# Performance work log

Hardware: AMD Instinct MI355X
Metric: run time of the kernel (lower is better)

The kernel has to match this reference:

```python
import jax, jax.numpy as jnp
import numpy as np

N = 50000
E = 800000
G = 2500  # number of graphs


def setup_inputs() -> dict:
    key = jax.random.key(0)
    ks = jax.random.split(key, 10)
    x = jax.random.normal(ks[0], (N, 128), dtype=jnp.float32)
    edge_index = jax.random.randint(ks[1], (2, E), 0, N, dtype=jnp.int64)
    batch = jnp.sort(jax.random.randint(ks[2], (N,), 0, G, dtype=jnp.int64))
    def lin(k, fan_in, shape):
        return jax.random.normal(k, shape, dtype=jnp.float32) / np.sqrt(fan_in)
    return {
        'x': x, 'edge_index': edge_index, 'batch': batch,
        'W1': lin(ks[3], 128, (128, 64)), 'b1': jnp.zeros((64,), jnp.float32),
        'W2': lin(ks[4], 64, (64, 64)),  'b2': jnp.zeros((64,), jnp.float32),
        'W3': lin(ks[5], 64, (64, 64)),  'b3': jnp.zeros((64,), jnp.float32),
        'Wp1': lin(ks[6], 64, (64, 64)), 'bp1': jnp.zeros((64,), jnp.float32),
        'Wp2': lin(ks[7], 64, (64, 32)), 'bp2': jnp.zeros((32,), jnp.float32),
    }


def _gcn_norm(edge_index, n_nodes):
    # PyG GCNConv default: add self-loops, symmetric normalization
    loops = jnp.arange(n_nodes, dtype=edge_index.dtype)
    src = jnp.concatenate([edge_index[0], loops])
    dst = jnp.concatenate([edge_index[1], loops])
    deg = jax.ops.segment_sum(jnp.ones_like(dst, dtype=jnp.float32), dst,
                              num_segments=n_nodes)
    dis = jnp.where(deg > 0, jax.lax.rsqrt(deg), 0.0)
    norm = dis[src] * dis[dst]  # [E + N]
    return src, dst, norm


def _gcn_conv(x, W, b, src, dst, norm, n_nodes):
    h = x @ W                                   # transform first (small dim)
    m = h[src] * norm[:, None]                  # gather + scale
    out = jax.ops.segment_sum(m, dst, num_segments=n_nodes)  # scatter-add
    return out + b


def reference(x, edge_index, batch, W1, b1, W2, b2, W3, b3, Wp1, bp1, Wp2, bp2):
    n_nodes = x.shape[0]
    src, dst, norm = _gcn_norm(edge_index, n_nodes)
    x1 = jax.nn.relu(_gcn_conv(x, W1, b1, src, dst, norm, n_nodes))
    x2 = jax.nn.relu(_gcn_conv(x1, W2, b2, src, dst, norm, n_nodes))
    x3 = jax.nn.relu(_gcn_conv(x2, W3, b3, src, dst, norm, n_nodes))
    h = x1 + x2 + x3
    # global_mean_pool
    sums = jax.ops.segment_sum(h, batch, num_segments=G)
    counts = jax.ops.segment_sum(jnp.ones((n_nodes,), jnp.float32), batch,
                                 num_segments=G)
    pooled = sums / jnp.maximum(counts, 1.0)[:, None]
    z = jax.nn.relu(pooled @ Wp1 + bp1) @ Wp2 + bp2
    return z
```

## Files before the change

### kernel.cpp

```cpp
#include <hip/hip_runtime.h>
#include <math.h>


typedef short short8 __attribute__((ext_vector_type(8)));
typedef float f32x4 __attribute__((ext_vector_type(4)));

__device__ inline float bf2f(unsigned short h) {
    return __uint_as_float((unsigned)h << 16);
}
__device__ inline unsigned short f2bf(float f) {
    unsigned u = __float_as_uint(f);
    return (unsigned short)((u + (0x7FFFu + ((u >> 16) & 1u))) >> 16);
}
__device__ inline unsigned short f2h(float f) {
    union { _Float16 h; unsigned short u; } c;
    c.h = (_Float16)f;
    return c.u;
}
__device__ inline float h2f(unsigned short u) {
    union { unsigned short u; _Float16 h; } c;
    c.u = u;
    return (float)c.h;
}
__device__ inline void bh8f(short8 u, float4& a, float4& b) {
    a.x = bf2f((unsigned short)u[0]); a.y = bf2f((unsigned short)u[1]);
    a.z = bf2f((unsigned short)u[2]); a.w = bf2f((unsigned short)u[3]);
    b.x = bf2f((unsigned short)u[4]); b.y = bf2f((unsigned short)u[5]);
    b.z = bf2f((unsigned short)u[6]); b.w = bf2f((unsigned short)u[7]);
}
__device__ inline float4 f4fma(float s, float4 a, float4 acc) {
    acc.x += s * a.x; acc.y += s * a.y; acc.z += s * a.z; acc.w += s * a.w;
    return acc;
}

template <int K>
__global__ __launch_bounds__(256) void k_hist_gemm(const int* __restrict__ dst,
                                                   int* __restrict__ hist, int E, int chunk,
                                                   const float* __restrict__ X,
                                                   const float* __restrict__ W,
                                                   unsigned short* __restrict__ H, int n) {
    __shared__ int hh[256];
    __shared__ short wt[64 * K];
    int t = threadIdx.x;
    if (blockIdx.x < 256) {
        hh[t] = 0;
        __syncthreads();
        int e0 = blockIdx.x * chunk;
        int e1 = min(e0 + chunk, E);
        for (int e = e0 + t; e < e1; e += 256) atomicAdd(&hh[dst[e] >> 8], 1);
        __syncthreads();
        hist[blockIdx.x * 256 + t] = hh[t];
        return;
    }
    for (int idx = t; idx < 64 * K; idx += 256) {
        int k = idx >> 6, ch = idx & 63;
        wt[ch * K + k] = (short)f2bf(W[idx]);
    }
    __syncthreads();
    int wave = t >> 6, lane = t & 63;
    int q = lane >> 4, l = lane & 15;
    int tile = (blockIdx.x - 256) * 4 + wave;
    if (tile * 16 >= n) return;
    int node = tile * 16 + l;
    short8 afr[4][K / 32];
#pragma unroll
    for (int mb = 0; mb < 4; mb++)
#pragma unroll
        for (int s = 0; s < K / 32; s++)
            afr[mb][s] = *(const short8*)(wt + (mb * 16 + l) * K + s * 32 + q * 8);
    f32x4 acc[4] = {};
    const float* xr = X + (size_t)node * K + q * 8;
#pragma unroll
    for (int s = 0; s < K / 32; s++) {
        float4 xa = *(const float4*)(xr + s * 32);
        float4 xb = *(const float4*)(xr + s * 32 + 4);
        short8 bfr;
        bfr[0] = (short)f2bf(xa.x); bfr[1] = (short)f2bf(xa.y);
        bfr[2] = (short)f2bf(xa.z); bfr[3] = (short)f2bf(xa.w);
        bfr[4] = (short)f2bf(xb.x); bfr[5] = (short)f2bf(xb.y);
        bfr[6] = (short)f2bf(xb.z); bfr[7] = (short)f2bf(xb.w);
#pragma unroll
        for (int mb = 0; mb < 4; mb++)
            acc[mb] = __builtin_amdgcn_mfma_f32_16x16x32_bf16(afr[mb][s], bfr, acc[mb], 0, 0, 0);
    }
#pragma unroll
    for (int mb = 0; mb < 4; mb++) {
        ushort4 u;
        u.x = f2bf(acc[mb][0]); u.y = f2bf(acc[mb][1]);
        u.z = f2bf(acc[mb][2]); u.w = f2bf(acc[mb][3]);
        ((ushort4*)H)[(size_t)node * 16 + mb * 4 + q] = u;
    }
}

__global__ void kA_colscan(const int* __restrict__ hist, int* __restrict__ cursorA,
                           int* __restrict__ tot) {
    __shared__ int s[256];
    int t = threadIdx.x;
    int k = blockIdx.x;
    int v = hist[t * 256 + k];
    s[t] = v;
    __syncthreads();
    for (int st = 1; st < 256; st <<= 1) {
        int u = s[t];
        if (t >= st) u += s[t - st];
        __syncthreads();
        s[t] = u;
        __syncthreads();
    }
    cursorA[t * 256 + k] = s[t] - v;
    if (t == 255) tot[k] = s[255];
}

__global__ void kA_scatter(const int* __restrict__ src, const int* __restrict__ dst,
                           const int* __restrict__ cursorA, const int* __restrict__ tot,
                           unsigned* __restrict__ ebuf, int E, int chunk) {
    __shared__ int s[256];
    __shared__ int cur[256];
    int t = threadIdx.x;
    s[t] = tot[t];
    __syncthreads();
    for (int st = 1; st < 256; st <<= 1) {
        int u = s[t];
        if (t >= st) u += s[t - st];
        __syncthreads();
        s[t] = u;
        __syncthreads();
    }
    int bstart = (t == 0) ? 0 : s[t - 1];
    cur[t] = cursorA[blockIdx.x * 256 + t] + bstart;
    __syncthreads();
    int e0 = blockIdx.x * chunk;
    int e1 = min(e0 + chunk, E);
    for (int e = e0 + t; e < e1; e += 256) {
        int d = dst[e];
        int p = atomicAdd(&cur[d >> 8], 1);
        ebuf[p] = ((unsigned)(d & 255) << 24) | (unsigned)src[e];
    }
}

__global__ void kB1(const unsigned* __restrict__ ebuf, const int* __restrict__ tot,
                    float* __restrict__ dis, int* __restrict__ offsP, int N) {
    __shared__ int s[256];
    __shared__ int h[256];
    int t = threadIdx.x;
    int k = blockIdx.x;
    s[t] = tot[t];
    __syncthreads();
    for (int st = 1; st < 256; st <<= 1) {
        int u = s[t];
        if (t >= st) u += s[t - st];
        __syncthreads();
        s[t] = u;
        __syncthreads();
    }
    int lo = (k == 0) ? 0 : s[k - 1];
    int hi = s[k];
    int padbase = lo + 768 * k;
    h[t] = 0;
    __syncthreads();
    for (int p = lo + t; p < hi; p += 256) atomicAdd(&h[ebuf[p] >> 24], 1);
    __syncthreads();
    int c = h[t];
    int cp = (c + 3) & ~3;
    int node = k * 256 + t;
    if (node < N) dis[node] = rsqrtf((float)(c + 1));
    s[t] = cp;
    __syncthreads();
    for (int st = 1; st < 256; st <<= 1) {
        int u = s[t];
        if (t >= st) u += s[t - st];
        __syncthreads();
        s[t] = u;
        __syncthreads();
    }
    if (node < N) offsP[node] = ((padbase + s[t] - cp) << 9) | cp;
}

__global__ void kB2(const unsigned* __restrict__ ebuf, const int* __restrict__ tot,
                    const float* __restrict__ dis, const int* __restrict__ offsP,
                    unsigned* __restrict__ col, int N) {
    __shared__ int s[256];
    __shared__ int cur[256];
    int t = threadIdx.x;
    int k = blockIdx.x;
    s[t] = tot[t];
    __syncthreads();
    for (int st = 1; st < 256; st <<= 1) {
        int u = s[t];
        if (t >= st) u += s[t - st];
        __syncthreads();
        s[t] = u;
        __syncthreads();
    }
    int lo = (k == 0) ? 0 : s[k - 1];
    int hi = s[k];
    int node = k * 256 + t;
    int po = (node < N) ? offsP[node] : 0;
    cur[t] = po >> 9;
    __syncthreads();
    for (int p = lo + t; p < hi; p += 256) {
        unsigned e = ebuf[p];
        int srcI = (int)(e & 0x00FFFFFFu);
        int q = atomicAdd(&cur[e >> 24], 1);
        col[q] = ((unsigned)f2h(dis[srcI]) << 16) | (unsigned)srcI;
    }
    __syncthreads();
    if (node < N) {
        int end = (po >> 9) + (po & 511);
        for (int q = cur[t]; q < end; q++) col[q] = 0u;
    }
}

__global__ __launch_bounds__(256) void k_aggemm(const unsigned short* __restrict__ H,
                                                const unsigned* __restrict__ col,
                                                const int* __restrict__ offsP,
                                                const float* __restrict__ dis,
                                                const float* __restrict__ bias,
                                                const float* __restrict__ W,
                                                unsigned short* __restrict__ Xout,
                                                unsigned short* __restrict__ Hout, int n) {
    __shared__ short wt[64 * 64];
    __shared__ short vbuf[64 * 72];
    int t = threadIdx.x;
    for (int idx = t; idx < 64 * 64; idx += 256) {
        int k = idx >> 6, ch = idx & 63;
        wt[ch * 64 + k] = (short)f2bf(W[idx]);
    }
    const short8* Hs = (const short8*)H;
    int base = blockIdx.x * 64;
    int cs = t & 7;
    const float4* bias4 = (const float4*)bias;
    float4 bb0 = bias4[cs * 2];
    float4 bb1 = bias4[cs * 2 + 1];
#pragma unroll
    for (int r = 0; r < 2; r++) {
        int nl = r * 32 + (t >> 3);
        int node = base + nl;
        if (node < n) {
            float dn = dis[node];
            float4 acc0, acc1;
            bh8f(Hs[(size_t)node * 8 + cs], acc0, acc1);
            acc0.x *= dn; acc0.y *= dn; acc0.z *= dn; acc0.w *= dn;
            acc1.x *= dn; acc1.y *= dn; acc1.z *= dn; acc1.w *= dn;
            int po = offsP[node];
            int p = po >> 9, hi = p + (po & 511);
            for (; p < hi; p += 4) {
                uint4 e4 = *(const uint4*)(col + p);
                short8 g0 = Hs[(size_t)(e4.x & 0xFFFFu) * 8 + cs];
                short8 g1 = Hs[(size_t)(e4.y & 0xFFFFu) * 8 + cs];
                short8 g2 = Hs[(size_t)(e4.z & 0xFFFFu) * 8 + cs];
                short8 g3 = Hs[(size_t)(e4.w & 0xFFFFu) * 8 + cs];
                float w0 = h2f((unsigned short)(e4.x >> 16));
                float w1 = h2f((unsigned short)(e4.y >> 16));
                float w2 = h2f((unsigned short)(e4.z >> 16));
                float w3 = h2f((unsigned short)(e4.w >> 16));
                float4 a, b;
                bh8f(g0, a, b); acc0 = f4fma(w0, a, acc0); acc1 = f4fma(w0, b, acc1);
                bh8f(g1, a, b); acc0 = f4fma(w1, a, acc0); acc1 = f4fma(w1, b, acc1);
                bh8f(g2, a, b); acc0 = f4fma(w2, a, acc0); acc1 = f4fma(w2, b, acc1);
                bh8f(g3, a, b); acc0 = f4fma(w3, a, acc0); acc1 = f4fma(w3, b, acc1);
            }
            float4 v0, v1;
            v0.x = fmaxf(acc0.x * dn + bb0.x, 0.f);
            v0.y = fmaxf(acc0.y * dn + bb0.y, 0.f);
            v0.z = fmaxf(acc0.z * dn + bb0.z, 0.f);
            v0.w = fmaxf(acc0.w * dn + bb0.w, 0.f);
            v1.x = fmaxf(acc1.x * dn + bb1.x, 0.f);
            v1.y = fmaxf(acc1.y * dn + bb1.y, 0.f);
            v1.z = fmaxf(acc1.z * dn + bb1.z, 0.f);
            v1.w = fmaxf(acc1.w * dn + bb1.w, 0.f);
            short8 o;
            o[0] = (short)f2bf(v0.x); o[1] = (short)f2bf(v0.y);
            o[2] = (short)f2bf(v0.z); o[3] = (short)f2bf(v0.w);
            o[4] = (short)f2bf(v1.x); o[5] = (short)f2bf(v1.y);
            o[6] = (short)f2bf(v1.z); o[7] = (short)f2bf(v1.w);
            ((short8*)Xout)[(size_t)node * 8 + cs] = o;
            *(short8*)(vbuf + nl * 72 + cs * 8) = o;
        }
    }
    __syncthreads();
    int wave = t >> 6, lane = t & 63;
    int q = lane >> 4, l = lane & 15;
    if (base + wave * 16 >= n) return;
    int node = base + wave * 16 + l;
    short8 afr[4][2];
#pragma unroll
    for (int mb = 0; mb < 4; mb++)
#pragma unroll
        for (int s = 0; s < 2; s++)
            afr[mb][s] = *(const short8*)(wt + (mb * 16 + l) * 64 + s * 32 + q * 8);
    f32x4 acc[4] = {};
#pragma unroll
    for (int s = 0; s < 2; s++) {
        short8 bfr = *(const short8*)(vbuf + (wave * 16 + l) * 72 + s * 32 + q * 8);
#pragma unroll
        for (int mb = 0; mb < 4; mb++)
            acc[mb] = __builtin_amdgcn_mfma_f32_16x16x32_bf16(afr[mb][s], bfr, acc[mb], 0, 0, 0);
    }
#pragma unroll
    for (int mb = 0; mb < 4; mb++) {
        ushort4 u;
        u.x = f2bf(acc[mb][0]); u.y = f2bf(acc[mb][1]);
        u.z = f2bf(acc[mb][2]); u.w = f2bf(acc[mb][3]);
        ((ushort4*)Hout)[(size_t)node * 16 + mb * 4 + q] = u;
    }
}

__global__ void k_agg3(const unsigned short* __restrict__ H, const unsigned* __restrict__ col,
                       const int* __restrict__ offsP, const float* __restrict__ dis,
                       const float* __restrict__ bias,
                       const unsigned short* __restrict__ add1,
                       const unsigned short* __restrict__ add2,
                       float* __restrict__ OutS, int n) {
    int t = threadIdx.x;
    int node = blockIdx.x * 32 + (t >> 3);
    if (node >= n) return;
    int lane = t & 7;
    const short8* Hs = (const short8*)H;
    float dn = dis[node];
    float4 acc0, acc1;
    bh8f(Hs[(size_t)node * 8 + lane], acc0, acc1);
    acc0.x *= dn; acc0.y *= dn; acc0.z *= dn; acc0.w *= dn;
    acc1.x *= dn; acc1.y *= dn; acc1.z *= dn; acc1.w *= dn;
    int po = offsP[node];
    int p = po >> 9, hi = p + (po & 511);
    for (; p < hi; p += 4) {
        uint4 e4 = *(const uint4*)(col + p);
        short8 g0 = Hs[(size_t)(e4.x & 0xFFFFu) * 8 + lane];
        short8 g1 = Hs[(size_t)(e4.y & 0xFFFFu) * 8 + lane];
        short8 g2 = Hs[(size_t)(e4.z & 0xFFFFu) * 8 + lane];
        short8 g3 = Hs[(size_t)(e4.w & 0xFFFFu) * 8 + lane];
        float w0 = h2f((unsigned short)(e4.x >> 16));
        float w1 = h2f((unsigned short)(e4.y >> 16));
        float w2 = h2f((unsigned short)(e4.z >> 16));
        float w3 = h2f((unsigned short)(e4.w >> 16));
        float4 a, b;
        bh8f(g0, a, b); acc0 = f4fma(w0, a, acc0); acc1 = f4fma(w0, b, acc1);
        bh8f(g1, a, b); acc0 = f4fma(w1, a, acc0); acc1 = f4fma(w1, b, acc1);
        bh8f(g2, a, b); acc0 = f4fma(w2, a, acc0); acc1 = f4fma(w2, b, acc1);
        bh8f(g3, a, b); acc0 = f4fma(w3, a, acc0); acc1 = f4fma(w3, b, acc1);
    }
    const float4* bias4 = (const float4*)bias;
    float4 bb0 = bias4[lane * 2];
    float4 bb1 = bias4[lane * 2 + 1];
    float4 v0, v1;
    v0.x = fmaxf(acc0.x * dn + bb0.x, 0.f);
    v0.y = fmaxf(acc0.y * dn + bb0.y, 0.f);
    v0.z = fmaxf(acc0.z * dn + bb0.z, 0.f);
    v0.w = fmaxf(acc0.w * dn + bb0.w, 0.f);
    v1.x = fmaxf(acc1.x * dn + bb1.x, 0.f);
    v1.y = fmaxf(acc1.y * dn + bb1.y, 0.f);
    v1.z = fmaxf(acc1.z * dn + bb1.z, 0.f);
    v1.w = fmaxf(acc1.w * dn + bb1.w, 0.f);
    size_t slot = (size_t)node * 8 + lane;
    float4 a10, a11, a20, a21;
    bh8f(((const short8*)add1)[slot], a10, a11);
    bh8f(((const short8*)add2)[slot], a20, a21);
    v0.x += a10.x + a20.x; v0.y += a10.y + a20.y;
    v0.z += a10.z + a20.z; v0.w += a10.w + a20.w;
    v1.x += a11.x + a21.x; v1.y += a11.y + a21.y;
    v1.z += a11.z + a21.z; v1.w += a11.w + a21.w;
    float4* S4 = (float4*)OutS;
    size_t oi = (size_t)node * 16 + (size_t)lane * 2;
    S4[oi] = v0;
    S4[oi + 1] = v1;
}

__global__ void k_poolhead(const float* __restrict__ S, const int* __restrict__ batch,
                           const float* __restrict__ Wp1, const float* __restrict__ bp1,
                           const float* __restrict__ Wp2, const float* __restrict__ bp2,
                           float* __restrict__ out, int n, int G) {
    int g = blockIdx.x;
    int j = threadIdx.x;
    int a = 0, b = n;
    while (a < b) { int m = (a + b) >> 1; if (batch[m] < g) a = m + 1; else b = m; }
    int beg = a;
    b = n;
    while (a < b) { int m = (a + b) >> 1; if (batch[m] < g + 1) a = m + 1; else b = m; }
    int end = a;
    float sum = 0.f;
    int i = beg;
    for (; i + 2 <= end; i += 2)
        sum += S[(size_t)i * 64 + j] + S[(size_t)(i + 1) * 64 + j];
    if (i < end) sum += S[(size_t)i * 64 + j];
    float cnt = (float)(end - beg);
    float p = sum / fmaxf(cnt, 1.f);
    __shared__ float ps[64];
    __shared__ float ts[64];
    ps[j] = p;
    __syncthreads();
    float t1 = bp1[j];
#pragma unroll 8
    for (int k = 0; k < 64; k++) t1 += ps[k] * Wp1[k * 64 + j];
    t1 = fmaxf(t1, 0.f);
    ts[j] = t1;
    __syncthreads();
    if (j < 32) {
        float o = bp2[j];
#pragma unroll 8
        for (int k = 0; k < 64; k++) o += ts[k] * Wp2[k * 32 + j];
        out[(size_t)g * 32 + j] = o;
    }
}

extern "C" void kernel_launch(void* const* d_in, const int* in_sizes, int n_in,
                              void* d_out, int out_size, void* d_ws, size_t ws_size,
                              hipStream_t stream) {
    const float* x   = (const float*)d_in[0];
    const int*   ei  = (const int*)d_in[1];
    const int*   bat = (const int*)d_in[2];
    const float* W1  = (const float*)d_in[3];
    const float* b1  = (const float*)d_in[4];
    const float* W2  = (const float*)d_in[5];
    const float* b2  = (const float*)d_in[6];
    const float* W3  = (const float*)d_in[7];
    const float* b3  = (const float*)d_in[8];
    const float* Wp1 = (const float*)d_in[9];
    const float* bp1 = (const float*)d_in[10];
    const float* Wp2 = (const float*)d_in[11];
    const float* bp2 = (const float*)d_in[12];

    int N = in_sizes[0] / 128;
    int E = in_sizes[1] / 2;
    int G = out_size / 32;
    const int* src = ei;
    const int* dst = ei + E;

    char* w = (char*)d_ws;
    auto alloc = [&](size_t bytes) -> void* {
        void* p = (void*)w;
        w += (bytes + 255) & ~(size_t)255;
        return p;
    };
    int NB = (N + 255) / 256;
    int*            offsP   = (int*)alloc((size_t)N * 4);
    unsigned*       col     = (unsigned*)alloc(((size_t)E + 3 * (size_t)N + 1024) * 4);
    float*          dis     = (float*)alloc((size_t)N * 4);
    int*            hist    = (int*)alloc((size_t)256 * 256 * 4);
    int*            cursorA = (int*)alloc((size_t)256 * 256 * 4);
    int*            tot     = (int*)alloc((size_t)256 * 4);
    unsigned*       ebuf    = (unsigned*)alloc((size_t)E * 4);
    unsigned short* Hb      = (unsigned short*)alloc((size_t)N * 64 * 2);
    unsigned short* Hb2     = (unsigned short*)alloc((size_t)N * 64 * 2);
    unsigned short* X1      = (unsigned short*)alloc((size_t)N * 64 * 2);
    unsigned short* X2      = (unsigned short*)alloc((size_t)N * 64 * 2);
    float*          S       = (float*)alloc((size_t)N * 64 * 4);

    int chunk = (E + 255) / 256;
    int ggemm = ((N >> 4) + 3) / 4;
    int gfuse = (N + 63) / 64;
    int gagg  = (N + 31) / 32;

    k_hist_gemm<128><<<256 + ggemm, 256, 0, stream>>>(dst, hist, E, chunk, x, W1, Hb, N);
    kA_colscan<<<256, 256, 0, stream>>>(hist, cursorA, tot);
    kA_scatter<<<256, 256, 0, stream>>>(src, dst, cursorA, tot, ebuf, E, chunk);
    kB1<<<NB, 256, 0, stream>>>(ebuf, tot, dis, offsP, N);
    kB2<<<NB, 256, 0, stream>>>(ebuf, tot, dis, offsP, col, N);

    k_aggemm<<<gfuse, 256, 0, stream>>>(Hb, col, offsP, dis, b1, W2, X1, Hb2, N);
    k_aggemm<<<gfuse, 256, 0, stream>>>(Hb2, col, offsP, dis, b2, W3, X2, Hb, N);
    k_agg3<<<gagg, 256, 0, stream>>>(Hb, col, offsP, dis, b3, X1, X2, S, N);

    k_poolhead<<<G, 64, 0, stream>>>(S, bat, Wp1, bp1, Wp2, bp2, (float*)d_out, N, G);
}
```

Measured before the change: 218.6 us.

## Fuse mean-pool summation into final aggregation via atomic adds per graph

The last GCN aggregation kernel no longer writes a full N x 64 fp32 node buffer. It atomically adds each node's features straight into a G x 64 per-graph sum buffer, which is zeroed inside the column-scan kernel. The pool/head kernel then only reads the per-graph sums and divides by the node count. This removes a large global write and re-read, but adds many float atomics that contend on the same graph rows, since sorted batch ids put neighbouring nodes in the same graph. Summation order also becomes nondeterministic.

```diff
diff --git a/kernel.cpp b/kernel.cpp
--- a/kernel.cpp
+++ b/kernel.cpp
@@ -93,10 +93,11 @@
 }
 
 __global__ void kA_colscan(const int* __restrict__ hist, int* __restrict__ cursorA,
-                           int* __restrict__ tot) {
+                           int* __restrict__ tot, float* __restrict__ P, int Pn) {
     __shared__ int s[256];
     int t = threadIdx.x;
     int k = blockIdx.x;
+    for (int i = k * 256 + t; i < Pn; i += 65536) P[i] = 0.f;
     int v = hist[t * 256 + k];
     s[t] = v;
     __syncthreads();
@@ -306,12 +307,13 @@
     }
 }
 
-__global__ void k_agg3(const unsigned short* __restrict__ H, const unsigned* __restrict__ col,
-                       const int* __restrict__ offsP, const float* __restrict__ dis,
-                       const float* __restrict__ bias,
-                       const unsigned short* __restrict__ add1,
-                       const unsigned short* __restrict__ add2,
-                       float* __restrict__ OutS, int n) {
+__global__ void k_agg3_pool(const unsigned short* __restrict__ H, const unsigned* __restrict__ col,
+                            const int* __restrict__ offsP, const float* __restrict__ dis,
+                            const float* __restrict__ bias,
+                            const unsigned short* __restrict__ add1,
+                            const unsigned short* __restrict__ add2,
+                            const int* __restrict__ batch,
+                            float* __restrict__ P, int n) {
     int t = threadIdx.x;
     int node = blockIdx.x * 32 + (t >> 3);
     if (node >= n) return;
@@ -360,13 +362,14 @@
     v0.z += a10.z + a20.z; v0.w += a10.w + a20.w;
     v1.x += a11.x + a21.x; v1.y += a11.y + a21.y;
     v1.z += a11.z + a21.z; v1.w += a11.w + a21.w;
-    float4* S4 = (float4*)OutS;
-    size_t oi = (size_t)node * 16 + (size_t)lane * 2;
-    S4[oi] = v0;
-    S4[oi + 1] = v1;
-}
-
-__global__ void k_poolhead(const float* __restrict__ S, const int* __restrict__ batch,
+    float* pg = P + (size_t)batch[node] * 64 + lane * 8;
+    atomicAdd(pg + 0, v0.x); atomicAdd(pg + 1, v0.y);
+    atomicAdd(pg + 2, v0.z); atomicAdd(pg + 3, v0.w);
+    atomicAdd(pg + 4, v1.x); atomicAdd(pg + 5, v1.y);
+    atomicAdd(pg + 6, v1.z); atomicAdd(pg + 7, v1.w);
+}
+
+__global__ void k_poolhead(const float* __restrict__ P, const int* __restrict__ batch,
                            const float* __restrict__ Wp1, const float* __restrict__ bp1,
                            const float* __restrict__ Wp2, const float* __restrict__ bp2,
                            float* __restrict__ out, int n, int G) {
@@ -378,13 +381,8 @@
     b = n;
     while (a < b) { int m = (a + b) >> 1; if (batch[m] < g + 1) a = m + 1; else b = m; }
     int end = a;
-    float sum = 0.f;
-    int i = beg;
-    for (; i + 2 <= end; i += 2)
-        sum += S[(size_t)i * 64 + j] + S[(size_t)(i + 1) * 64 + j];
-    if (i < end) sum += S[(size_t)i * 64 + j];
     float cnt = (float)(end - beg);
-    float p = sum / fmaxf(cnt, 1.f);
+    float p = P[(size_t)g * 64 + j] / fmaxf(cnt, 1.f);
     __shared__ float ps[64];
     __shared__ float ts[64];
     ps[j] = p;
@@ -444,7 +442,7 @@
     unsigned short* Hb2     = (unsigned short*)alloc((size_t)N * 64 * 2);
     unsigned short* X1      = (unsigned short*)alloc((size_t)N * 64 * 2);
     unsigned short* X2      = (unsigned short*)alloc((size_t)N * 64 * 2);
-    float*          S       = (float*)alloc((size_t)N * 64 * 4);
+    float*          P       = (float*)alloc((size_t)G * 64 * 4);
 
     int chunk = (E + 255) / 256;
     int ggemm = ((N >> 4) + 3) / 4;
@@ -452,14 +450,14 @@
     int gagg  = (N + 31) / 32;
 
     k_hist_gemm<128><<<256 + ggemm, 256, 0, stream>>>(dst, hist, E, chunk, x, W1, Hb, N);
-    kA_colscan<<<256, 256, 0, stream>>>(hist, cursorA, tot);
+    kA_colscan<<<256, 256, 0, stream>>>(hist, cursorA, tot, P, G * 64);
     kA_scatter<<<256, 256, 0, stream>>>(src, dst, cursorA, tot, ebuf, E, chunk);
     kB1<<<NB, 256, 0, stream>>>(ebuf, tot, dis, offsP, N);
     kB2<<<NB, 256, 0, stream>>>(ebuf, tot, dis, offsP, col, N);
 
     k_aggemm<<<gfuse, 256, 0, stream>>>(Hb, col, offsP, dis, b1, W2, X1, Hb2, N);
     k_aggemm<<<gfuse, 256, 0, stream>>>(Hb2, col, offsP, dis, b2, W3, X2, Hb, N);
-    k_agg3<<<gagg, 256, 0, stream>>>(Hb, col, offsP, dis, b3, X1, X2, S, N);
-
-    k_poolhead<<<G, 64, 0, stream>>>(S, bat, Wp1, bp1, Wp2, bp2, (float*)d_out, N, G);
-}
+    k_agg3_pool<<<gagg, 256, 0, stream>>>(Hb, col, offsP, dis, b3, X1, X2, bat, P, N);
+
+    k_poolhead<<<G, 64, 0, stream>>>(P, bat, Wp1, bp1, Wp2, bp2, (float*)d_out, N, G);
+}
```

After: 342.7 us. +56.7%, slower.
